# Optimization experiments

Hardware: AMD Instinct MI355X
Metric: run time of the kernel (lower is better)

The kernel has to match this reference:

```python
import jax, jax.numpy as jnp
import numpy as np

B, S, D = 2, 2048, 1024
H = 16
HS = D // H  # head_size = 64
SCALE = HS ** 0.5


def setup_inputs() -> dict:
    key = jax.random.key(0)
    ks = jax.random.split(key, 7)
    std = 1.0 / np.sqrt(D)
    return {
        "x": jax.random.normal(ks[0], (B, S, D), dtype=jnp.float32),
        "Wq": jax.random.normal(ks[1], (D, D), dtype=jnp.float32) * std,
        "bq": jax.random.normal(ks[2], (D,), dtype=jnp.float32) * std,
        "Wk": jax.random.normal(ks[3], (D, D), dtype=jnp.float32) * std,
        "bk": jax.random.normal(ks[4], (D,), dtype=jnp.float32) * std,
        "Wv": jax.random.normal(ks[5], (D, D), dtype=jnp.float32) * std,
        "bv": jax.random.normal(ks[6], (D,), dtype=jnp.float32) * std,
    }


def reference(x, Wq, bq, Wk, bk, Wv, bv):
    bs, seq, _ = x.shape
    # QKV projections (torch Linear: x @ W.T + b)
    Q = (x @ Wq.T + bq).reshape(bs, seq, H, HS)
    K = (x @ Wk.T + bk).reshape(bs, seq, H, HS)
    V = (x @ Wv.T + bv).reshape(bs, seq, H, HS)
    # scores[b,h,q,k] = Q . K / scale
    scores = jnp.einsum("bqhd,bkhd->bhqk", Q, K) / SCALE
    # causal mask: disallow k > q
    causal = jnp.triu(jnp.ones((seq, seq), dtype=bool), k=1)
    scores = jnp.where(causal, -jnp.inf, scores)
    probs = jax.nn.softmax(scores, axis=-1)
    att = jnp.einsum("bhqk,bkhd->bqhd", probs, V)
    return att.reshape(bs, seq, H * HS)
```

## Files before the change

### kernel.cpp

```cpp
#include <hip/hip_runtime.h>

typedef unsigned short ushort_t;
typedef __bf16 bf16x8 __attribute__((ext_vector_type(8)));
typedef unsigned short ushortx8 __attribute__((ext_vector_type(8)));
typedef unsigned short ushortx4 __attribute__((ext_vector_type(4)));
typedef unsigned int uintx4 __attribute__((ext_vector_type(4)));
typedef float floatx4 __attribute__((ext_vector_type(4)));

__device__ inline void load16_lds(const ushort_t* g, ushort_t* l) {
  __builtin_amdgcn_global_load_lds(
      (__attribute__((address_space(1))) void*)(g),
      (__attribute__((address_space(3))) void*)(l),
      16, 0, 0);
}

__device__ inline float bf2f(ushort_t u) {
  unsigned int v = ((unsigned int)u) << 16;
  return __builtin_bit_cast(float, v);
}

__device__ inline ushort_t f2bf(float f) {
  unsigned int u = __builtin_bit_cast(unsigned int, f);
  u += 0x7fffu + ((u >> 16) & 1u);
  return (ushort_t)(u >> 16);
}

__device__ inline bf16x8 ldfrag(const ushort_t* p) {
  return __builtin_bit_cast(bf16x8, *(const ushortx8*)p);
}

__device__ inline bool sniff_f32(const ushort_t* x, int lane_off) {
  float v = fabsf(bf2f(x[lane_off]));
  bool big = !(v < 1e4f);
  return __ballot(big) != 0ull;
}

__global__ __launch_bounds__(256) void convert_all(
    const void* __restrict__ x,
    const void* __restrict__ wq, const void* __restrict__ wk, const void* __restrict__ wv,
    const void* __restrict__ bq, const void* __restrict__ bk, const void* __restrict__ bv,
    ushort_t* __restrict__ xb, ushort_t* __restrict__ wqb,
    ushort_t* __restrict__ wkb, ushort_t* __restrict__ wvb,
    float* __restrict__ biasf, int* __restrict__ flag)
{
  const bool f32 = sniff_f32((const ushort_t*)x, (int)(threadIdx.x & 63));
  const int seg = blockIdx.y;
  if (seg == 4) {
    if (blockIdx.x == 0 && threadIdx.x == 0) *flag = f32 ? 1 : 0;
    const int i = blockIdx.x * 256 + threadIdx.x;
    if (i >= 1024) return;
    const void* bs[3] = {bq, bk, bv};
#pragma unroll
    for (int k = 0; k < 3; ++k)
      biasf[k * 1024 + i] = f32 ? ((const float*)bs[k])[i] : bf2f(((const ushort_t*)bs[k])[i]);
    return;
  }
  const void* src = (seg == 0) ? x : (seg == 1) ? wq : (seg == 2) ? wk : wv;
  ushort_t* dst   = (seg == 0) ? xb : (seg == 1) ? wqb : (seg == 2) ? wkb : wvb;
  const int n = (seg == 0) ? 4194304 : 1048576;
  const int i = (blockIdx.x * 256 + threadIdx.x) * 8;
  if (i >= n) return;
  if (f32) {
    const float* s = (const float*)src + i;
    ushortx8 o;
#pragma unroll
    for (int j = 0; j < 8; ++j) o[j] = f2bf(s[j]);
    *(ushortx8*)(dst + i) = o;
  } else {
    *(ushortx8*)(dst + i) = *(const ushortx8*)((const ushort_t*)src + i);
  }
}

__global__ __launch_bounds__(256, 2) void qkv_gemm(
    const ushort_t* __restrict__ x,
    const ushort_t* __restrict__ Wq, const ushort_t* __restrict__ Wk,
    const ushort_t* __restrict__ Wv, const float* __restrict__ biasf,
    ushort_t* __restrict__ Qo, ushort_t* __restrict__ Ko, ushort_t* __restrict__ Vt)
{
  __shared__ __attribute__((aligned(16))) ushort_t As[128 * 32];
  __shared__ __attribute__((aligned(16))) ushort_t Bs[128 * 32];

  const int which = blockIdx.z;
  const ushort_t* W = (which == 0) ? Wq : (which == 1) ? Wk : Wv;
  const float oscale = (which == 0) ? 0.18033688011112042f : 1.0f;

  const int n0 = blockIdx.x * 128;
  const int m0 = blockIdx.y * 128;

  const int tid  = threadIdx.x;
  const int wave = tid >> 6;
  const int lane = tid & 63;
  const int ln   = lane & 15;
  const int quad = lane >> 4;
  const int wm = (wave >> 1) * 64;
  const int wn = (wave & 1) * 64;

  floatx4 acc[4][4];
#pragma unroll
  for (int i = 0; i < 4; ++i)
#pragma unroll
    for (int j = 0; j < 4; ++j) acc[i][j] = floatx4{0.f, 0.f, 0.f, 0.f};

  const int c1 = tid, c2 = tid + 256;
  const ushort_t* ga1 = x + (m0 + (c1 >> 2)) * 1024 + (c1 & 3) * 8;
  const ushort_t* ga2 = x + (m0 + (c2 >> 2)) * 1024 + (c2 & 3) * 8;
  const ushort_t* gb1 = W + (n0 + (c1 >> 2)) * 1024 + (c1 & 3) * 8;
  const ushort_t* gb2 = W + (n0 + (c2 >> 2)) * 1024 + (c2 & 3) * 8;
  ushort_t* la1 = As + wave * 512;
  ushort_t* la2 = As + 2048 + wave * 512;
  ushort_t* lb1 = Bs + wave * 512;
  ushort_t* lb2 = Bs + 2048 + wave * 512;

  for (int kt = 0; kt < 1024; kt += 32) {
    __syncthreads();
    load16_lds(ga1 + kt, la1);
    load16_lds(ga2 + kt, la2);
    load16_lds(gb1 + kt, lb1);
    load16_lds(gb2 + kt, lb2);
    __syncthreads();

    bf16x8 af[4], bfr[4];
#pragma unroll
    for (int mi = 0; mi < 4; ++mi)
      af[mi] = ldfrag(As + (wm + mi * 16 + ln) * 32 + quad * 8);
#pragma unroll
    for (int ni = 0; ni < 4; ++ni)
      bfr[ni] = ldfrag(Bs + (wn + ni * 16 + ln) * 32 + quad * 8);
#pragma unroll
    for (int mi = 0; mi < 4; ++mi)
#pragma unroll
      for (int ni = 0; ni < 4; ++ni)
        acc[mi][ni] = __builtin_amdgcn_mfma_f32_16x16x32_bf16(af[mi], bfr[ni], acc[mi][ni], 0, 0, 0);
  }

  float bvv[4];
#pragma unroll
  for (int ni = 0; ni < 4; ++ni) bvv[ni] = biasf[which * 1024 + n0 + wn + ni * 16 + ln];

  if (which == 2) {
#pragma unroll
    for (int mi = 0; mi < 4; ++mi)
#pragma unroll
      for (int ni = 0; ni < 4; ++ni) {
        const int col = n0 + wn + ni * 16 + ln;
        const int row0 = m0 + wm + mi * 16 + quad * 4;
        const int b = row0 >> 11, s0 = row0 & 2047;
        const int h = col >> 6, hs = col & 63;
        ushortx4 pk;
#pragma unroll
        for (int r = 0; r < 4; ++r) pk[r] = f2bf(acc[mi][ni][r] + bvv[ni]);
        *(ushortx4*)(Vt + ((size_t)((b * 16 + h) * 64 + hs)) * 2048 + s0) = pk;
      }
  } else {
    ushort_t* out = (which == 0) ? Qo : Ko;
#pragma unroll
    for (int mi = 0; mi < 4; ++mi)
#pragma unroll
      for (int ni = 0; ni < 4; ++ni) {
        const int col = n0 + wn + ni * 16 + ln;
#pragma unroll
        for (int r = 0; r < 4; ++r) {
          const int row = m0 + wm + mi * 16 + quad * 4 + r;
          out[row * 1024 + col] = f2bf((acc[mi][ni][r] + bvv[ni]) * oscale);
        }
      }
  }
}

__global__ __launch_bounds__(128) void flash12(
    const ushort_t* __restrict__ Q, const ushort_t* __restrict__ Kx,
    const ushort_t* __restrict__ Vt, void* __restrict__ out,
    const int* __restrict__ flag)
{
  __shared__ __attribute__((aligned(16))) float Cb[64][68];
  __shared__ float lbuf[64][4];

  const bool f32o = (*flag != 0);
  const int tid  = threadIdx.x;
  const int wave = tid >> 6;
  const int lane = tid & 63;
  const int ln = lane & 15, quad = lane >> 4;

  const int idxA = (ln + 32 * (quad & 1)) * 4;
  const int idxB = idxA + 64;
  const bool hiq = (quad >> 1) != 0;

  const int i = blockIdx.x;
  const int xcd = i & 7, j = i >> 3;
  const int bh = xcd * 4 + (j & 3);
  const int cc = 31 - (j >> 2);
  const int b = bh >> 4, h = bh & 15;
  const int qw = cc * 64;
  const int ntiles = cc + 1;

  const ushort_t* kbase = Kx + ((size_t)b * 2048) * 1024 + h * 64;
  const ushort_t* vbase = Vt + (size_t)bh * 64 * 2048;

  bf16x8 qf[4][2];
#pragma unroll
  for (int bi = 0; bi < 4; ++bi)
#pragma unroll
    for (int ks = 0; ks < 2; ++ks)
      qf[bi][ks] = ldfrag(Q + (size_t)(b * 2048 + qw + bi * 16 + ln) * 1024 + h * 64 + ks * 32 + quad * 8);

  floatx4 ot[4][4];
#pragma unroll
  for (int ai = 0; ai < 4; ++ai)
#pragma unroll
    for (int bi = 0; bi < 4; ++bi) ot[ai][bi] = floatx4{0.f, 0.f, 0.f, 0.f};
  float li[4] = {0.f, 0.f, 0.f, 0.f};

  bf16x8 kf0[4][2], kf1[4][2], vf[4][2];

#define LOADK(KF, KV0) do {                                                   \
    const ushort_t* kp_ = kbase + (size_t)((KV0) + ln) * 1024 + quad * 8;     \
    _Pragma("unroll")                                                         \
    for (int mi_ = 0; mi_ < 4; ++mi_) {                                       \
      KF[mi_][0] = ldfrag(kp_ + mi_ * 16384);                                 \
      KF[mi_][1] = ldfrag(kp_ + mi_ * 16384 + 32);                            \
    }                                                                         \
  } while (0)

#define LOADV(KV0) do {                                                       \
    const ushort_t* vp_ = vbase + (size_t)ln * 2048 + (KV0) + quad * 8;       \
    _Pragma("unroll")                                                         \
    for (int ai_ = 0; ai_ < 4; ++ai_) {                                       \
      vf[ai_][0] = ldfrag(vp_ + ai_ * 32768);                                 \
      vf[ai_][1] = ldfrag(vp_ + ai_ * 32768 + 32);                            \
    }                                                                         \
  } while (0)

#define TILE(KF, T) do {                                                      \
    const int kv0_ = (T) * 64;                                                \
    const bool diag_ = ((T) == ntiles - 1);                                   \
    _Pragma("unroll")                                                         \
    for (int bi = 0; bi < 4; ++bi) {                                          \
      floatx4 st[4];                                                          \
      _Pragma("unroll")                                                       \
      for (int mi = 0; mi < 4; ++mi) st[mi] = floatx4{0.f, 0.f, 0.f, 0.f};    \
      _Pragma("unroll")                                                       \
      for (int mi = 0; mi < 4; ++mi) {                                        \
        st[mi] = __builtin_amdgcn_mfma_f32_16x16x32_bf16(KF[mi][0], qf[bi][0], st[mi], 0, 0, 0); \
        st[mi] = __builtin_amdgcn_mfma_f32_16x16x32_bf16(KF[mi][1], qf[bi][1], st[mi], 0, 0, 0); \
      }                                                                       \
      const int qrow_ = qw + bi * 16 + ln;                                    \
      float p[4][4];                                                          \
      if (diag_) {                                                            \
        _Pragma("unroll")                                                     \
        for (int mi = 0; mi < 4; ++mi)                                        \
          _Pragma("unroll")                                                   \
          for (int r = 0; r < 4; ++r) {                                       \
            const int kv_ = kv0_ + mi * 16 + quad * 4 + r;                    \
            const float e_ = __builtin_amdgcn_exp2f(st[mi][r]);               \
            p[mi][r] = (kv_ > qrow_) ? 0.f : e_;                              \
          }                                                                   \
      } else {                                                                \
        _Pragma("unroll")                                                     \
        for (int mi = 0; mi < 4; ++mi)                                        \
          _Pragma("unroll")                                                   \
          for (int r = 0; r < 4; ++r) p[mi][r] = __builtin_amdgcn_exp2f(st[mi][r]); \
      }                                                                       \
      unsigned d[4][2];                                                       \
      _Pragma("unroll")                                                       \
      for (int mi = 0; mi < 4; ++mi) {                                        \
        li[bi] += (p[mi][0] + p[mi][1]) + (p[mi][2] + p[mi][3]);              \
        d[mi][0] = __builtin_amdgcn_perm(                                     \
            __builtin_bit_cast(unsigned, p[mi][1]), __builtin_bit_cast(unsigned, p[mi][0]), 0x07060302u); \
        d[mi][1] = __builtin_amdgcn_perm(                                     \
            __builtin_bit_cast(unsigned, p[mi][3]), __builtin_bit_cast(unsigned, p[mi][2]), 0x07060302u); \
      }                                                                       \
      bf16x8 pb[2];                                                           \
      _Pragma("unroll")                                                       \
      for (int ks = 0; ks < 2; ++ks) {                                        \
        uintx4 w;                                                             \
        _Pragma("unroll")                                                     \
        for (int jj = 0; jj < 4; ++jj) {                                      \
          const int idx_ = (jj >> 1) ? idxB : idxA;                           \
          const int lo_ = __builtin_amdgcn_ds_bpermute(idx_, (int)d[2 * ks][jj & 1]);     \
          const int hi_ = __builtin_amdgcn_ds_bpermute(idx_, (int)d[2 * ks + 1][jj & 1]); \
          w[jj] = (unsigned)(hiq ? hi_ : lo_);                                \
        }                                                                     \
        pb[ks] = __builtin_bit_cast(bf16x8, w);                               \
      }                                                                       \
      _Pragma("unroll")                                                       \
      for (int ai = 0; ai < 4; ++ai) {                                        \
        ot[ai][bi] = __builtin_amdgcn_mfma_f32_16x16x32_bf16(vf[ai][0], pb[0], ot[ai][bi], 0, 0, 0); \
        ot[ai][bi] = __builtin_amdgcn_mfma_f32_16x16x32_bf16(vf[ai][1], pb[1], ot[ai][bi], 0, 0, 0); \
      }                                                                       \
    }                                                                         \
  } while (0)

  int t = wave;
  if (t < ntiles) LOADK(kf0, t * 64);
  for (; t < ntiles; t += 4) {
    LOADV(t * 64);
    if (t + 2 < ntiles) LOADK(kf1, (t + 2) * 64);
    TILE(kf0, t);
    if (t + 2 < ntiles) {
      LOADV((t + 2) * 64);
      if (t + 4 < ntiles) LOADK(kf0, (t + 4) * 64);
      TILE(kf1, t + 2);
    }
  }

#undef LOADK
#undef LOADV
#undef TILE

  if (wave == 1) {
#pragma unroll
    for (int bi = 0; bi < 4; ++bi) {
#pragma unroll
      for (int ai = 0; ai < 4; ++ai)
        *(floatx4*)&Cb[bi * 16 + ln][ai * 16 + quad * 4] = ot[ai][bi];
    }
#pragma unroll
    for (int bi = 0; bi < 4; ++bi) lbuf[lane][bi] = li[bi];
  }
  __syncthreads();
  if (wave == 0) {
#pragma unroll
    for (int bi = 0; bi < 4; ++bi) {
#pragma unroll
      for (int ai = 0; ai < 4; ++ai) {
        const floatx4 o = *(const floatx4*)&Cb[bi * 16 + ln][ai * 16 + quad * 4];
#pragma unroll
        for (int r = 0; r < 4; ++r) ot[ai][bi][r] += o[r];
      }
      li[bi] += lbuf[lane][bi];
    }

#pragma unroll
    for (int bi = 0; bi < 4; ++bi) {
      li[bi] += __shfl_xor(li[bi], 16);
      li[bi] += __shfl_xor(li[bi], 32);
      const float inv = 1.0f / li[bi];
      const int qrow = qw + bi * 16 + ln;
      if (f32o) {
        float* of = (float*)out;
#pragma unroll
        for (int ai = 0; ai < 4; ++ai) {
          floatx4 o;
#pragma unroll
          for (int r = 0; r < 4; ++r) o[r] = ot[ai][bi][r] * inv;
          *(floatx4*)(of + (size_t)(b * 2048 + qrow) * 1024 + h * 64 + ai * 16 + quad * 4) = o;
        }
      } else {
        ushort_t* ob = (ushort_t*)out;
#pragma unroll
        for (int ai = 0; ai < 4; ++ai) {
          ushortx4 pk;
#pragma unroll
          for (int r = 0; r < 4; ++r) pk[r] = f2bf(ot[ai][bi][r] * inv);
          *(ushortx4*)(ob + (size_t)(b * 2048 + qrow) * 1024 + h * 64 + ai * 16 + quad * 4) = pk;
        }
      }
    }
  }
}

extern "C" void kernel_launch(void* const* d_in, const int* in_sizes, int n_in,
                              void* d_out, int out_size, void* d_ws, size_t ws_size,
                              hipStream_t stream) {
  char* w = (char*)d_ws;
  int* flag = (int*)w;
  size_t off = 256;
  ushort_t* xb  = (ushort_t*)(w + off); off += (size_t)4194304 * 2;
  ushort_t* wqb = (ushort_t*)(w + off); off += (size_t)1048576 * 2;
  ushort_t* wkb = (ushort_t*)(w + off); off += (size_t)1048576 * 2;
  ushort_t* wvb = (ushort_t*)(w + off); off += (size_t)1048576 * 2;
  float* biasf  = (float*)(w + off);    off += (size_t)3 * 1024 * 4;
  ushort_t* Qw  = (ushort_t*)(w + off); off += (size_t)4194304 * 2;
  ushort_t* Kw  = (ushort_t*)(w + off); off += (size_t)4194304 * 2;
  ushort_t* Vtw = (ushort_t*)(w + off);

  convert_all<<<dim3(2048, 5), 256, 0, stream>>>(
      d_in[0], d_in[1], d_in[3], d_in[5], d_in[2], d_in[4], d_in[6],
      xb, wqb, wkb, wvb, biasf, flag);
  qkv_gemm<<<dim3(8, 32, 3), 256, 0, stream>>>(xb, wqb, wkb, wvb, biasf, Qw, Kw, Vtw);
  flash12<<<1024, 128, 0, stream>>>(Qw, Kw, Vtw, d_out, flag);
}
```

Baseline: 164.0 us.

## Switch flash attention to 32x32x16 MFMA with permlane-based P repacking

Rewrites the attention kernel to use 32x32x16 bf16 MFMA tiles instead of 16x16x32, changing the fragment layouts for Q, K, V and the output accumulators. The probability tile is converted with v_cvt_pk_bf16_f32 and rearranged with v_permlane32_swap instead of ds_bpermute shuffles, which removes LDS-path permutes from the inner loop. It also adds a min-blocks occupancy hint of 2. The cost is that output stores become scalar per element rather than vectorized, and the larger accumulators add register pressure.

```diff
diff --git a/kernel.cpp b/kernel.cpp
--- a/kernel.cpp
+++ b/kernel.cpp
@@ -6,6 +6,7 @@
 typedef unsigned short ushortx4 __attribute__((ext_vector_type(4)));
 typedef unsigned int uintx4 __attribute__((ext_vector_type(4)));
 typedef float floatx4 __attribute__((ext_vector_type(4)));
+typedef float floatx16 __attribute__((ext_vector_type(16)));
 
 __device__ inline void load16_lds(const ushort_t* g, ushort_t* l) {
   __builtin_amdgcn_global_load_lds(
@@ -27,6 +28,16 @@
 
 __device__ inline bf16x8 ldfrag(const ushort_t* p) {
   return __builtin_bit_cast(bf16x8, *(const ushortx8*)p);
+}
+
+__device__ inline unsigned cvtpk_bf16(float lo, float hi) {
+  unsigned r;
+  asm("v_cvt_pk_bf16_f32 %0, %1, %2" : "=v"(r) : "v"(lo), "v"(hi));
+  return r;
+}
+
+__device__ inline void plswap(unsigned& a, unsigned& b) {
+  asm("v_permlane32_swap_b32 %0, %1" : "+v"(a), "+v"(b));
 }
 
 __device__ inline bool sniff_f32(const ushort_t* x, int lane_off) {
@@ -167,23 +178,23 @@
   }
 }
 
-__global__ __launch_bounds__(128) void flash12(
+__global__ __launch_bounds__(128, 2) void flash13(
     const ushort_t* __restrict__ Q, const ushort_t* __restrict__ Kx,
     const ushort_t* __restrict__ Vt, void* __restrict__ out,
     const int* __restrict__ flag)
 {
   __shared__ __attribute__((aligned(16))) float Cb[64][68];
-  __shared__ float lbuf[64][4];
+  __shared__ float lbufW[64];
+  __shared__ float ILi[64];
 
   const bool f32o = (*flag != 0);
   const int tid  = threadIdx.x;
   const int wave = tid >> 6;
   const int lane = tid & 63;
-  const int ln = lane & 15, quad = lane >> 4;
-
-  const int idxA = (ln + 32 * (quad & 1)) * 4;
-  const int idxB = idxA + 64;
-  const bool hiq = (quad >> 1) != 0;
+  const int l31 = lane & 31;
+  const int hi  = lane >> 5;
+
+#define CROW(r) (((r) & 3) + 8 * ((r) >> 2) + 4 * hi)
 
   const int i = blockIdx.x;
   const int xcd = i & 7, j = i >> 3;
@@ -196,167 +207,164 @@
   const ushort_t* kbase = Kx + ((size_t)b * 2048) * 1024 + h * 64;
   const ushort_t* vbase = Vt + (size_t)bh * 64 * 2048;
 
-  bf16x8 qf[4][2];
-#pragma unroll
-  for (int bi = 0; bi < 4; ++bi)
-#pragma unroll
-    for (int ks = 0; ks < 2; ++ks)
-      qf[bi][ks] = ldfrag(Q + (size_t)(b * 2048 + qw + bi * 16 + ln) * 1024 + h * 64 + ks * 32 + quad * 8);
-
-  floatx4 ot[4][4];
-#pragma unroll
-  for (int ai = 0; ai < 4; ++ai)
-#pragma unroll
-    for (int bi = 0; bi < 4; ++bi) ot[ai][bi] = floatx4{0.f, 0.f, 0.f, 0.f};
-  float li[4] = {0.f, 0.f, 0.f, 0.f};
-
-  bf16x8 kf0[4][2], kf1[4][2], vf[4][2];
+  bf16x8 qf[2][4];
+#pragma unroll
+  for (int qq = 0; qq < 2; ++qq)
+#pragma unroll
+    for (int s = 0; s < 4; ++s)
+      qf[qq][s] = ldfrag(Q + (size_t)(b * 2048 + qw + 32 * qq + l31) * 1024 + h * 64 + s * 16 + hi * 8);
+
+  floatx16 ot[2][2];
+#pragma unroll
+  for (int qq = 0; qq < 2; ++qq)
+#pragma unroll
+    for (int dq = 0; dq < 2; ++dq)
+#pragma unroll
+      for (int r = 0; r < 16; ++r) ot[qq][dq][r] = 0.f;
+  float li[2] = {0.f, 0.f};
+
+  bf16x8 kfA[8], kfB[8], vf[8];
 
 #define LOADK(KF, KV0) do {                                                   \
-    const ushort_t* kp_ = kbase + (size_t)((KV0) + ln) * 1024 + quad * 8;     \
-    _Pragma("unroll")                                                         \
-    for (int mi_ = 0; mi_ < 4; ++mi_) {                                       \
-      KF[mi_][0] = ldfrag(kp_ + mi_ * 16384);                                 \
-      KF[mi_][1] = ldfrag(kp_ + mi_ * 16384 + 32);                            \
-    }                                                                         \
+    const ushort_t* kp_ = kbase + (size_t)((KV0) + l31) * 1024 + hi * 8;      \
+    KF[0] = ldfrag(kp_);       KF[1] = ldfrag(kp_ + 16);                      \
+    KF[2] = ldfrag(kp_ + 32);  KF[3] = ldfrag(kp_ + 48);                      \
+    const ushort_t* kq_ = kp_ + 32 * 1024;                                    \
+    KF[4] = ldfrag(kq_);       KF[5] = ldfrag(kq_ + 16);                      \
+    KF[6] = ldfrag(kq_ + 32);  KF[7] = ldfrag(kq_ + 48);                      \
   } while (0)
 
 #define LOADV(KV0) do {                                                       \
-    const ushort_t* vp_ = vbase + (size_t)ln * 2048 + (KV0) + quad * 8;       \
-    _Pragma("unroll")                                                         \
-    for (int ai_ = 0; ai_ < 4; ++ai_) {                                       \
-      vf[ai_][0] = ldfrag(vp_ + ai_ * 32768);                                 \
-      vf[ai_][1] = ldfrag(vp_ + ai_ * 32768 + 32);                            \
-    }                                                                         \
+    const ushort_t* vp0_ = vbase + (size_t)l31 * 2048 + (KV0) + hi * 8;       \
+    vf[0] = ldfrag(vp0_);       vf[1] = ldfrag(vp0_ + 16);                    \
+    vf[2] = ldfrag(vp0_ + 32);  vf[3] = ldfrag(vp0_ + 48);                    \
+    const ushort_t* vp1_ = vp0_ + (size_t)32 * 2048;                          \
+    vf[4] = ldfrag(vp1_);       vf[5] = ldfrag(vp1_ + 16);                    \
+    vf[6] = ldfrag(vp1_ + 32);  vf[7] = ldfrag(vp1_ + 48);                    \
   } while (0)
 
-#define TILE(KF, T) do {                                                      \
+#define PACK_PV(PARR, SH, SIDX, QQ) do {                                      \
+    unsigned X_ = cvtpk_bf16(PARR[8 * (SH) + 0], PARR[8 * (SH) + 1]);         \
+    unsigned Y_ = cvtpk_bf16(PARR[8 * (SH) + 2], PARR[8 * (SH) + 3]);         \
+    unsigned Z_ = cvtpk_bf16(PARR[8 * (SH) + 4], PARR[8 * (SH) + 5]);         \
+    unsigned W_ = cvtpk_bf16(PARR[8 * (SH) + 6], PARR[8 * (SH) + 7]);         \
+    plswap(X_, Z_);                                                           \
+    plswap(Y_, W_);                                                           \
+    uintx4 u_ = {X_, Y_, Z_, W_};                                             \
+    const bf16x8 pa_ = __builtin_bit_cast(bf16x8, u_);                        \
+    ot[QQ][0] = __builtin_amdgcn_mfma_f32_32x32x16_bf16(pa_, vf[(SIDX)], ot[QQ][0], 0, 0, 0);     \
+    ot[QQ][1] = __builtin_amdgcn_mfma_f32_32x32x16_bf16(pa_, vf[4 + (SIDX)], ot[QQ][1], 0, 0, 0); \
+  } while (0)
+
+#define TILE32(KF, T) do {                                                    \
     const int kv0_ = (T) * 64;                                                \
     const bool diag_ = ((T) == ntiles - 1);                                   \
     _Pragma("unroll")                                                         \
-    for (int bi = 0; bi < 4; ++bi) {                                          \
-      floatx4 st[4];                                                          \
+    for (int qq = 0; qq < 2; ++qq) {                                          \
+      floatx16 st0, st1;                                                      \
       _Pragma("unroll")                                                       \
-      for (int mi = 0; mi < 4; ++mi) st[mi] = floatx4{0.f, 0.f, 0.f, 0.f};    \
+      for (int r = 0; r < 16; ++r) { st0[r] = 0.f; st1[r] = 0.f; }            \
       _Pragma("unroll")                                                       \
-      for (int mi = 0; mi < 4; ++mi) {                                        \
-        st[mi] = __builtin_amdgcn_mfma_f32_16x16x32_bf16(KF[mi][0], qf[bi][0], st[mi], 0, 0, 0); \
-        st[mi] = __builtin_amdgcn_mfma_f32_16x16x32_bf16(KF[mi][1], qf[bi][1], st[mi], 0, 0, 0); \
+      for (int s = 0; s < 4; ++s) {                                           \
+        st0 = __builtin_amdgcn_mfma_f32_32x32x16_bf16(KF[s], qf[qq][s], st0, 0, 0, 0);     \
+        st1 = __builtin_amdgcn_mfma_f32_32x32x16_bf16(KF[4 + s], qf[qq][s], st1, 0, 0, 0); \
       }                                                                       \
-      const int qrow_ = qw + bi * 16 + ln;                                    \
-      float p[4][4];                                                          \
+      float p0[16], p1[16];                                                   \
       if (diag_) {                                                            \
+        const int qg_ = qw + 32 * qq + l31;                                   \
         _Pragma("unroll")                                                     \
-        for (int mi = 0; mi < 4; ++mi)                                        \
-          _Pragma("unroll")                                                   \
-          for (int r = 0; r < 4; ++r) {                                       \
-            const int kv_ = kv0_ + mi * 16 + quad * 4 + r;                    \
-            const float e_ = __builtin_amdgcn_exp2f(st[mi][r]);               \
-            p[mi][r] = (kv_ > qrow_) ? 0.f : e_;                              \
-          }                                                                   \
+        for (int r = 0; r < 16; ++r) {                                        \
+          const int kva_ = kv0_ + CROW(r);                                    \
+          const float e0_ = __builtin_amdgcn_exp2f(st0[r]);                   \
+          const float e1_ = __builtin_amdgcn_exp2f(st1[r]);                   \
+          p0[r] = (kva_ > qg_) ? 0.f : e0_;                                   \
+          p1[r] = (kva_ + 32 > qg_) ? 0.f : e1_;                              \
+        }                                                                     \
       } else {                                                                \
         _Pragma("unroll")                                                     \
-        for (int mi = 0; mi < 4; ++mi)                                        \
-          _Pragma("unroll")                                                   \
-          for (int r = 0; r < 4; ++r) p[mi][r] = __builtin_amdgcn_exp2f(st[mi][r]); \
+        for (int r = 0; r < 16; ++r) {                                        \
+          p0[r] = __builtin_amdgcn_exp2f(st0[r]);                             \
+          p1[r] = __builtin_amdgcn_exp2f(st1[r]);                             \
+        }                                                                     \
       }                                                                       \
-      unsigned d[4][2];                                                       \
+      float ls_ = 0.f;                                                        \
       _Pragma("unroll")                                                       \
-      for (int mi = 0; mi < 4; ++mi) {                                        \
-        li[bi] += (p[mi][0] + p[mi][1]) + (p[mi][2] + p[mi][3]);              \
-        d[mi][0] = __builtin_amdgcn_perm(                                     \
-            __builtin_bit_cast(unsigned, p[mi][1]), __builtin_bit_cast(unsigned, p[mi][0]), 0x07060302u); \
-        d[mi][1] = __builtin_amdgcn_perm(                                     \
-            __builtin_bit_cast(unsigned, p[mi][3]), __builtin_bit_cast(unsigned, p[mi][2]), 0x07060302u); \
-      }                                                                       \
-      bf16x8 pb[2];                                                           \
-      _Pragma("unroll")                                                       \
-      for (int ks = 0; ks < 2; ++ks) {                                        \
-        uintx4 w;                                                             \
-        _Pragma("unroll")                                                     \
-        for (int jj = 0; jj < 4; ++jj) {                                      \
-          const int idx_ = (jj >> 1) ? idxB : idxA;                           \
-          const int lo_ = __builtin_amdgcn_ds_bpermute(idx_, (int)d[2 * ks][jj & 1]);     \
-          const int hi_ = __builtin_amdgcn_ds_bpermute(idx_, (int)d[2 * ks + 1][jj & 1]); \
-          w[jj] = (unsigned)(hiq ? hi_ : lo_);                                \
-        }                                                                     \
-        pb[ks] = __builtin_bit_cast(bf16x8, w);                               \
-      }                                                                       \
-      _Pragma("unroll")                                                       \
-      for (int ai = 0; ai < 4; ++ai) {                                        \
-        ot[ai][bi] = __builtin_amdgcn_mfma_f32_16x16x32_bf16(vf[ai][0], pb[0], ot[ai][bi], 0, 0, 0); \
-        ot[ai][bi] = __builtin_amdgcn_mfma_f32_16x16x32_bf16(vf[ai][1], pb[1], ot[ai][bi], 0, 0, 0); \
-      }                                                                       \
+      for (int r = 0; r < 16; ++r) ls_ += p0[r] + p1[r];                      \
+      li[qq] += ls_;                                                          \
+      PACK_PV(p0, 0, 0, qq);                                                  \
+      PACK_PV(p0, 1, 1, qq);                                                  \
+      PACK_PV(p1, 0, 2, qq);                                                  \
+      PACK_PV(p1, 1, 3, qq);                                                  \
     }                                                                         \
   } while (0)
 
   int t = wave;
-  if (t < ntiles) LOADK(kf0, t * 64);
+  if (t < ntiles) LOADK(kfA, t * 64);
   for (; t < ntiles; t += 4) {
     LOADV(t * 64);
-    if (t + 2 < ntiles) LOADK(kf1, (t + 2) * 64);
-    TILE(kf0, t);
+    if (t + 2 < ntiles) LOADK(kfB, (t + 2) * 64);
+    TILE32(kfA, t);
     if (t + 2 < ntiles) {
       LOADV((t + 2) * 64);
-      if (t + 4 < ntiles) LOADK(kf0, (t + 4) * 64);
-      TILE(kf1, t + 2);
+      if (t + 4 < ntiles) LOADK(kfA, (t + 4) * 64);
+      TILE32(kfB, t + 2);
     }
   }
 
 #undef LOADK
 #undef LOADV
-#undef TILE
+#undef PACK_PV
+#undef TILE32
+
+  float lf[2];
+#pragma unroll
+  for (int qq = 0; qq < 2; ++qq) lf[qq] = li[qq] + __shfl_xor(li[qq], 32);
 
   if (wave == 1) {
 #pragma unroll
-    for (int bi = 0; bi < 4; ++bi) {
-#pragma unroll
-      for (int ai = 0; ai < 4; ++ai)
-        *(floatx4*)&Cb[bi * 16 + ln][ai * 16 + quad * 4] = ot[ai][bi];
+    for (int qq = 0; qq < 2; ++qq) {
+#pragma unroll
+      for (int dq = 0; dq < 2; ++dq)
+#pragma unroll
+        for (int r = 0; r < 16; ++r)
+          Cb[32 * qq + CROW(r)][32 * dq + l31] = ot[qq][dq][r];
+      lbufW[32 * qq + l31] = lf[qq];
     }
-#pragma unroll
-    for (int bi = 0; bi < 4; ++bi) lbuf[lane][bi] = li[bi];
   }
   __syncthreads();
   if (wave == 0) {
 #pragma unroll
-    for (int bi = 0; bi < 4; ++bi) {
-#pragma unroll
-      for (int ai = 0; ai < 4; ++ai) {
-        const floatx4 o = *(const floatx4*)&Cb[bi * 16 + ln][ai * 16 + quad * 4];
-#pragma unroll
-        for (int r = 0; r < 4; ++r) ot[ai][bi][r] += o[r];
-      }
-      li[bi] += lbuf[lane][bi];
+    for (int qq = 0; qq < 2; ++qq) {
+#pragma unroll
+      for (int dq = 0; dq < 2; ++dq)
+#pragma unroll
+        for (int r = 0; r < 16; ++r)
+          ot[qq][dq][r] += Cb[32 * qq + CROW(r)][32 * dq + l31];
+      lf[qq] += lbufW[32 * qq + l31];
+      ILi[32 * qq + l31] = 1.0f / lf[qq];
     }
 
 #pragma unroll
-    for (int bi = 0; bi < 4; ++bi) {
-      li[bi] += __shfl_xor(li[bi], 16);
-      li[bi] += __shfl_xor(li[bi], 32);
-      const float inv = 1.0f / li[bi];
-      const int qrow = qw + bi * 16 + ln;
-      if (f32o) {
-        float* of = (float*)out;
-#pragma unroll
-        for (int ai = 0; ai < 4; ++ai) {
-          floatx4 o;
-#pragma unroll
-          for (int r = 0; r < 4; ++r) o[r] = ot[ai][bi][r] * inv;
-          *(floatx4*)(of + (size_t)(b * 2048 + qrow) * 1024 + h * 64 + ai * 16 + quad * 4) = o;
-        }
-      } else {
-        ushort_t* ob = (ushort_t*)out;
-#pragma unroll
-        for (int ai = 0; ai < 4; ++ai) {
-          ushortx4 pk;
-#pragma unroll
-          for (int r = 0; r < 4; ++r) pk[r] = f2bf(ot[ai][bi][r] * inv);
-          *(ushortx4*)(ob + (size_t)(b * 2048 + qrow) * 1024 + h * 64 + ai * 16 + quad * 4) = pk;
+    for (int qq = 0; qq < 2; ++qq) {
+#pragma unroll
+      for (int r = 0; r < 16; ++r) {
+        const int q_ = qw + 32 * qq + CROW(r);
+        const float iv = ILi[32 * qq + CROW(r)];
+        if (f32o) {
+          float* of = (float*)out;
+#pragma unroll
+          for (int dq = 0; dq < 2; ++dq)
+            of[(size_t)(b * 2048 + q_) * 1024 + h * 64 + 32 * dq + l31] = ot[qq][dq][r] * iv;
+        } else {
+          ushort_t* ob = (ushort_t*)out;
+#pragma unroll
+          for (int dq = 0; dq < 2; ++dq)
+            ob[(size_t)(b * 2048 + q_) * 1024 + h * 64 + 32 * dq + l31] = f2bf(ot[qq][dq][r] * iv);
         }
       }
     }
   }
+#undef CROW
 }
 
 extern "C" void kernel_launch(void* const* d_in, const int* in_sizes, int n_in,
@@ -378,5 +386,5 @@
       d_in[0], d_in[1], d_in[3], d_in[5], d_in[2], d_in[4], d_in[6],
       xb, wqb, wkb, wvb, biasf, flag);
   qkv_gemm<<<dim3(8, 32, 3), 256, 0, stream>>>(xb, wqb, wkb, wvb, biasf, Qw, Kw, Vtw);
-  flash12<<<1024, 128, 0, stream>>>(Qw, Kw, Vtw, d_out, flag);
-}
+  flash13<<<1024, 128, 0, stream>>>(Qw, Kw, Vtw, d_out, flag);
+}
```

New measurement: 205.3 us. +25.2%, slower.
